# Performance work log

Measured on AMD Instinct MI355X. Metric: run time of the kernel, lower is better.

The kernel has to match this reference:

```python
import jax, jax.numpy as jnp
import numpy as np

NUM_AGES = 100
FEAT_DIM = 512
BATCH = 4096
TEMPERATURE = 0.1
EPS = 1e-6


def setup_inputs() -> dict:
    key = jax.random.key(0)
    k1, k2, k3 = jax.random.split(key, 3)
    z_age = jax.random.normal(k1, (BATCH, FEAT_DIM), dtype=jnp.float32)
    ages = jax.random.randint(k2, (BATCH,), 0, NUM_AGES, dtype=jnp.int64)
    proxies = jax.random.normal(k3, (NUM_AGES, FEAT_DIM), dtype=jnp.float32)
    return {"z_age": z_age, "ages": ages, "proxies": proxies}


def _unit_diff(a, b):
    d = a - b
    return d / (jnp.linalg.norm(d, axis=-1, keepdims=True) + EPS)


def reference(z_age, ages, proxies):
    # Vectorized equivalent of the O(B^2) python double loop.
    # Only pairs with age_i < age_j contribute (age_i > age_j branch is a no-op `...`).
    B = z_age.shape[0]
    A = proxies.shape[0]
    aj = ages.astype(jnp.int32)
    c_cur = proxies[aj]                                   # [B, D]
    c_next = proxies[jnp.minimum(aj + 1, A - 1)]          # [B, D]
    c_prev = proxies[jnp.maximum(aj - 1, 0)]              # [B, D]
    vf = _unit_diff(c_next, c_cur)                        # forward direction per sample j
    vb = _unit_diff(c_prev, c_cur)                        # backward direction per sample j

    # Pairwise norms via Gram matrix: ||z_i - z_j||.
    G = z_age @ z_age.T                                   # [B, B]
    sq = jnp.diagonal(G)                                  # [B]
    d2 = jnp.maximum(sq[:, None] + sq[None, :] - 2.0 * G, 0.0)
    norm = jnp.sqrt(d2)                                   # [B, B]
    denom = norm + EPS

    # dot(v_d_ij, v_f_j) = (z_i . vf_j - z_j . vf_j) / (||z_i - z_j|| + eps)
    Gf = z_age @ vf.T                                     # [B, B], Gf[i, j] = z_i . vf_j
    Gb = z_age @ vb.T
    dot_f = (Gf - jnp.diagonal(Gf)[None, :]) / denom
    dot_b = (Gb - jnp.diagonal(Gb)[None, :]) / denom

    # -log(exp(df/T) / (exp(df/T) + exp(db/T))) = softplus((db - df)/T)
    per_pair = jax.nn.softplus((dot_b - dot_f) / TEMPERATURE)  # [B, B]
    mask = ages[:, None] < ages[None, :]
    loss = jnp.sum(jnp.where(mask, per_pair, 0.0))
    return loss / (B * (B - 1))
```

## Files before the change

### kernel.cpp

```cpp
#include <hip/hip_runtime.h>
#include <hip/hip_bf16.h>

#define NUM_AGES 100
#define FEAT 512
#define BATCH 4096
#define EPSF 1e-6f
#define INV_T 10.0f
#define INV_NORM (1.0f / ((float)BATCH * (float)(BATCH - 1)))

#define BM 128
#define BN 128
#define BK 64
#define NTILES 528

typedef __bf16 bf16_t;
typedef __bf16 v8bf __attribute__((ext_vector_type(8)));
typedef float v4f __attribute__((ext_vector_type(4)));

__device__ __forceinline__ void async16(const void* g, void* l) {
  __builtin_amdgcn_global_load_lds(
      (const __attribute__((address_space(1))) void*)g,
      (__attribute__((address_space(3))) void*)l, 16, 0, 0);
}

__global__ __launch_bounds__(512) void prep_kernel(
    const float* __restrict__ z, const int* __restrict__ ages,
    const float* __restrict__ proxies,
    bf16_t* __restrict__ zb, bf16_t* __restrict__ wb,
    float* __restrict__ sq, float* __restrict__ hd,
    int* __restrict__ ages_s, float* __restrict__ out)
{
  __shared__ __attribute__((aligned(16))) int sa[BATCH];
  int t = threadIdx.x;
  int wv = t >> 6, lane = t & 63;
  if (blockIdx.x == 0 && t == 0) out[0] = 0.0f;

  ((int4*)sa)[t]       = ((const int4*)ages)[t];
  ((int4*)sa)[t + 512] = ((const int4*)ages)[t + 512];
  __syncthreads();

  int j = blockIdx.x * 8 + wv;
  int araw = sa[j];

  int cnt = 0;
  const int4* sa4 = (const int4*)sa;
#pragma unroll
  for (int e = 0; e < 16; ++e) {
    int idx = lane + 64 * e;
    int4 v = sa4[idx];
    int k = idx * 4;
    cnt += (v.x < araw || (v.x == araw && k     < j)) ? 1 : 0;
    cnt += (v.y < araw || (v.y == araw && k + 1 < j)) ? 1 : 0;
    cnt += (v.z < araw || (v.z == araw && k + 2 < j)) ? 1 : 0;
    cnt += (v.w < araw || (v.w == araw && k + 3 < j)) ? 1 : 0;
  }

  int a  = araw < 0 ? 0 : (araw > NUM_AGES - 1 ? NUM_AGES - 1 : araw);
  int an = a + 1 > NUM_AGES - 1 ? NUM_AGES - 1 : a + 1;
  int ap = a - 1 < 0 ? 0 : a - 1;
  int c0 = lane * 8;
  const float4* cc4 = (const float4*)(proxies + (size_t)a  * FEAT + c0);
  const float4* cn4 = (const float4*)(proxies + (size_t)an * FEAT + c0);
  const float4* cp4 = (const float4*)(proxies + (size_t)ap * FEAT + c0);
  const float4* zr4 = (const float4*)(z + (size_t)j * FEAT + c0);

  float zv[8], df[8], db[8];
  float ff = 0.f, bb = 0.f, zz = 0.f, zf = 0.f, zbs = 0.f;
#pragma unroll
  for (int h = 0; h < 2; ++h) {
    float4 c4 = cc4[h], n4 = cn4[h], p4 = cp4[h], z4 = zr4[h];
    float cA[4] = {c4.x, c4.y, c4.z, c4.w};
    float nA[4] = {n4.x, n4.y, n4.z, n4.w};
    float pA[4] = {p4.x, p4.y, p4.z, p4.w};
    float zA[4] = {z4.x, z4.y, z4.z, z4.w};
#pragma unroll
    for (int i2 = 0; i2 < 4; ++i2) {
      int i = h * 4 + i2;
      zv[i] = zA[i2];
      df[i] = nA[i2] - cA[i2];
      db[i] = pA[i2] - cA[i2];
      ff  += df[i] * df[i];
      bb  += db[i] * db[i];
      zz  += zv[i] * zv[i];
      zf  += zv[i] * df[i];
      zbs += zv[i] * db[i];
    }
  }

#pragma unroll
  for (int off = 32; off > 0; off >>= 1) {
    ff  += __shfl_xor(ff,  off, 64);
    bb  += __shfl_xor(bb,  off, 64);
    zz  += __shfl_xor(zz,  off, 64);
    zf  += __shfl_xor(zf,  off, 64);
    zbs += __shfl_xor(zbs, off, 64);
    cnt += __shfl_xor(cnt, off, 64);
  }
  int rank = cnt;
  float rf = 1.0f / (sqrtf(ff) + EPSF);
  float rb = 1.0f / (sqrtf(bb) + EPSF);
  int key = rank & 7;
  int c2s = (c0 & ~63) | ((((c0 >> 3) & 7) ^ key) << 3);

  union { bf16_t h[8]; uint4 u; } uz, uw;
#pragma unroll
  for (int i = 0; i < 8; ++i) {
    uz.h[i] = (bf16_t)zv[i];
    uw.h[i] = (bf16_t)(db[i] * rb - df[i] * rf);
  }
  *(uint4*)((char*)zb + ((size_t)rank * FEAT + c2s) * 2) = uz.u;
  *(uint4*)((char*)wb + ((size_t)rank * FEAT + c2s) * 2) = uw.u;
  if (lane == 0) {
    sq[rank] = zz;
    hd[rank] = rb * zbs - rf * zf;
    ages_s[rank] = araw;
  }
}

__global__ __launch_bounds__(256, 2) void pair_kernel(
    const bf16_t* __restrict__ zb, const bf16_t* __restrict__ wb,
    const float* __restrict__ sq, const float* __restrict__ hd,
    const int* __restrict__ ages, float* __restrict__ out)
{
  __shared__ __attribute__((aligned(16))) char lds[49152];
  __shared__ float s_sqi[BM];
  __shared__ int   s_agei[BM];
  __shared__ float s_sqj[BN];
  __shared__ float s_hdj[BN];
  __shared__ int   s_agej[BN];
  __shared__ float wsum[4];

  int t = threadIdx.x;
  int wv = t >> 6, lane = t & 63;

  int id = (blockIdx.x & 7) * (NTILES / 8) + (blockIdx.x >> 3);
  int bx = 0, rem = id;
  while (rem >= bx + 1) { rem -= bx + 1; ++bx; }
  int by = rem;
  int i0 = by * BM, j0 = bx * BN;

  if (t < BM) {
    s_sqi[t] = sq[i0 + t];
    s_agei[t] = ages[i0 + t];
  } else {
    int u = t - BM;
    s_sqj[u] = sq[j0 + u];
    s_hdj[u] = hd[j0 + u];
    s_agej[u] = ages[j0 + u];
  }

  v4f accG[4][4], accH[4][4];
#pragma unroll
  for (int a = 0; a < 4; ++a)
#pragma unroll
    for (int b = 0; b < 4; ++b) {
      accG[a][b] = (v4f){0.f, 0.f, 0.f, 0.f};
      accH[a][b] = (v4f){0.f, 0.f, 0.f, 0.f};
    }

  int wm = wv >> 1, wn = wv & 1;
  int lm = lane & 15, q = lane >> 4;
  int psw0 = ((q    ) ^ (lm & 7)) * 16;
  int psw1 = ((q + 4) ^ (lm & 7)) * 16;

  int loff = (lane >> 3) * FEAT + (lane & 7) * 8;
  const bf16_t* baseA = zb + (size_t)i0 * FEAT + loff;
  const bf16_t* baseZ = zb + (size_t)j0 * FEAT + loff;
  const bf16_t* baseW = wb + (size_t)j0 * FEAT + loff;

  for (int k0 = 0; k0 < FEAT; k0 += BK) {
#pragma unroll
    for (int c = 0; c < 4; ++c) {
      int chunk = wv * 4 + c;
      async16(baseA + (size_t)chunk * 8 * FEAT + k0, lds + chunk * 1024);
      async16(baseZ + (size_t)chunk * 8 * FEAT + k0, lds + 16384 + chunk * 1024);
      async16(baseW + (size_t)chunk * 8 * FEAT + k0, lds + 32768 + chunk * 1024);
    }
    __syncthreads();

#pragma unroll
    for (int s = 0; s < 2; ++s) {
      int psw = s ? psw1 : psw0;
      v8bf afr[4], bz[4], bw[4];
#pragma unroll
      for (int mi = 0; mi < 4; ++mi) {
        int r = wm * 64 + mi * 16 + lm;
        afr[mi] = *(const v8bf*)(lds + r * 128 + psw);
      }
#pragma unroll
      for (int ni = 0; ni < 4; ++ni) {
        int r = wn * 64 + ni * 16 + lm;
        bz[ni] = *(const v8bf*)(lds + 16384 + r * 128 + psw);
        bw[ni] = *(const v8bf*)(lds + 32768 + r * 128 + psw);
      }
#pragma unroll
      for (int mi = 0; mi < 4; ++mi)
#pragma unroll
        for (int ni = 0; ni < 4; ++ni) {
          accG[mi][ni] = __builtin_amdgcn_mfma_f32_16x16x32_bf16(afr[mi], bz[ni], accG[mi][ni], 0, 0, 0);
          accH[mi][ni] = __builtin_amdgcn_mfma_f32_16x16x32_bf16(afr[mi], bw[ni], accH[mi][ni], 0, 0, 0);
        }
    }
    __syncthreads();
  }

  float tsum = 0.f;
#pragma unroll
  for (int ni = 0; ni < 4; ++ni) {
    int jl = wn * 64 + ni * 16 + lm;
    float sqj = s_sqj[jl];
    float hdj = s_hdj[jl];
    int aj = s_agej[jl];
#pragma unroll
    for (int mi = 0; mi < 4; ++mi) {
#pragma unroll
      for (int r = 0; r < 4; ++r) {
        int il = wm * 64 + mi * 16 + q * 4 + r;
        float g = accG[mi][ni][r];
        float h = accH[mi][ni][r];
        float d2 = fmaxf(s_sqi[il] + sqj - 2.0f * g, 1e-12f);
        float rs = __builtin_amdgcn_rsqf(d2);
        float arg = (h - hdj) * INV_T * rs;
        float sp = fmaxf(arg, 0.0f) + __logf(1.0f + __expf(-fabsf(arg)));
        tsum += (s_agei[il] < aj) ? sp : 0.0f;
      }
    }
  }

#pragma unroll
  for (int off = 32; off > 0; off >>= 1) tsum += __shfl_down(tsum, off, 64);
  if (lane == 0) wsum[wv] = tsum;
  __syncthreads();
  if (t == 0)
    atomicAdd(out, (wsum[0] + wsum[1] + wsum[2] + wsum[3]) * INV_NORM);
}

extern "C" void kernel_launch(void* const* d_in, const int* in_sizes, int n_in,
                              void* d_out, int out_size, void* d_ws, size_t ws_size,
                              hipStream_t stream) {
  const float* z = (const float*)d_in[0];
  const int* ages = (const int*)d_in[1];
  const float* proxies = (const float*)d_in[2];
  float* out = (float*)d_out;

  char* ws = (char*)d_ws;
  bf16_t* zb = (bf16_t*)ws;
  bf16_t* wb = (bf16_t*)(ws + (size_t)4 * 1024 * 1024);
  size_t o = (size_t)8 * 1024 * 1024;
  float* sq      = (float*)(ws + o);
  float* hd      = (float*)(ws + o + 16384);
  int*   ages_s  = (int*)  (ws + o + 32768);

  prep_kernel<<<BATCH / 8, 512, 0, stream>>>(z, ages, proxies, zb, wb, sq, hd, ages_s, out);
  pair_kernel<<<NTILES, 256, 0, stream>>>(zb, wb, sq, hd, ages_s, out);
}
```

Measured before the change: 102.0 us.

## Replace per-sample direction GEMM with small per-age projection table

The second GEMM against per-sample direction vectors is replaced by a small GEMM of z against the 100 per-age direction vectors (padded to 128), producing a [128 x B] fp32 table. The pair kernel then does only the Gram GEMM and looks up h values from that table in its epilogue. This halves MFMA work and LDS traffic in the pair kernel and lets it use fewer registers, allowing 3 blocks per CU. In exchange it adds an extra kernel launch and scattered global reads of the table in the epilogue.

```diff
diff --git a/kernel.cpp b/kernel.cpp
--- a/kernel.cpp
+++ b/kernel.cpp
@@ -12,6 +12,7 @@
 #define BN 128
 #define BK 64
 #define NTILES 528
+#define UROWS 128
 
 typedef __bf16 bf16_t;
 typedef __bf16 v8bf __attribute__((ext_vector_type(8)));
@@ -26,13 +27,59 @@
 __global__ __launch_bounds__(512) void prep_kernel(
     const float* __restrict__ z, const int* __restrict__ ages,
     const float* __restrict__ proxies,
-    bf16_t* __restrict__ zb, bf16_t* __restrict__ wb,
-    float* __restrict__ sq, float* __restrict__ hd,
-    int* __restrict__ ages_s, float* __restrict__ out)
+    bf16_t* __restrict__ zb, bf16_t* __restrict__ ub,
+    float* __restrict__ sq, int* __restrict__ ages_s, float* __restrict__ out)
 {
-  __shared__ __attribute__((aligned(16))) int sa[BATCH];
   int t = threadIdx.x;
   int wv = t >> 6, lane = t & 63;
+
+  if (blockIdx.x >= 512) {
+    int a = (blockIdx.x - 512) * 8 + wv;
+    int c0 = lane * 8;
+    union { bf16_t h[8]; uint4 u; } uw;
+    if (a < NUM_AGES) {
+      int an = a + 1 > NUM_AGES - 1 ? NUM_AGES - 1 : a + 1;
+      int ap = a - 1 < 0 ? 0 : a - 1;
+      const float4* cc4 = (const float4*)(proxies + (size_t)a  * FEAT + c0);
+      const float4* cn4 = (const float4*)(proxies + (size_t)an * FEAT + c0);
+      const float4* cp4 = (const float4*)(proxies + (size_t)ap * FEAT + c0);
+      float df[8], db[8];
+      float ff = 0.f, bb = 0.f;
+#pragma unroll
+      for (int h = 0; h < 2; ++h) {
+        float4 c4 = cc4[h], n4 = cn4[h], p4 = cp4[h];
+        float cA[4] = {c4.x, c4.y, c4.z, c4.w};
+        float nA[4] = {n4.x, n4.y, n4.z, n4.w};
+        float pA[4] = {p4.x, p4.y, p4.z, p4.w};
+#pragma unroll
+        for (int i2 = 0; i2 < 4; ++i2) {
+          int i = h * 4 + i2;
+          df[i] = nA[i2] - cA[i2];
+          db[i] = pA[i2] - cA[i2];
+          ff += df[i] * df[i];
+          bb += db[i] * db[i];
+        }
+      }
+#pragma unroll
+      for (int off = 32; off > 0; off >>= 1) {
+        ff += __shfl_xor(ff, off, 64);
+        bb += __shfl_xor(bb, off, 64);
+      }
+      float rf = 1.0f / (sqrtf(ff) + EPSF);
+      float rb = 1.0f / (sqrtf(bb) + EPSF);
+#pragma unroll
+      for (int i = 0; i < 8; ++i)
+        uw.h[i] = (bf16_t)(db[i] * rb - df[i] * rf);
+    } else {
+      uw.u = (uint4){0u, 0u, 0u, 0u};
+    }
+    int key = a & 7;
+    int c2s = (c0 & ~63) | ((((c0 >> 3) & 7) ^ key) << 3);
+    *(uint4*)((char*)ub + ((size_t)a * FEAT + c2s) * 2) = uw.u;
+    return;
+  }
+
+  __shared__ __attribute__((aligned(16))) int sa[BATCH];
   if (blockIdx.x == 0 && t == 0) out[0] = 0.0f;
 
   ((int4*)sa)[t]       = ((const int4*)ages)[t];
@@ -55,74 +102,110 @@
     cnt += (v.w < araw || (v.w == araw && k + 3 < j)) ? 1 : 0;
   }
 
-  int a  = araw < 0 ? 0 : (araw > NUM_AGES - 1 ? NUM_AGES - 1 : araw);
-  int an = a + 1 > NUM_AGES - 1 ? NUM_AGES - 1 : a + 1;
-  int ap = a - 1 < 0 ? 0 : a - 1;
   int c0 = lane * 8;
-  const float4* cc4 = (const float4*)(proxies + (size_t)a  * FEAT + c0);
-  const float4* cn4 = (const float4*)(proxies + (size_t)an * FEAT + c0);
-  const float4* cp4 = (const float4*)(proxies + (size_t)ap * FEAT + c0);
   const float4* zr4 = (const float4*)(z + (size_t)j * FEAT + c0);
-
-  float zv[8], df[8], db[8];
-  float ff = 0.f, bb = 0.f, zz = 0.f, zf = 0.f, zbs = 0.f;
+  float zv[8];
+  float zz = 0.f;
 #pragma unroll
   for (int h = 0; h < 2; ++h) {
-    float4 c4 = cc4[h], n4 = cn4[h], p4 = cp4[h], z4 = zr4[h];
-    float cA[4] = {c4.x, c4.y, c4.z, c4.w};
-    float nA[4] = {n4.x, n4.y, n4.z, n4.w};
-    float pA[4] = {p4.x, p4.y, p4.z, p4.w};
+    float4 z4 = zr4[h];
     float zA[4] = {z4.x, z4.y, z4.z, z4.w};
 #pragma unroll
     for (int i2 = 0; i2 < 4; ++i2) {
-      int i = h * 4 + i2;
-      zv[i] = zA[i2];
-      df[i] = nA[i2] - cA[i2];
-      db[i] = pA[i2] - cA[i2];
-      ff  += df[i] * df[i];
-      bb  += db[i] * db[i];
-      zz  += zv[i] * zv[i];
-      zf  += zv[i] * df[i];
-      zbs += zv[i] * db[i];
-    }
-  }
-
+      zv[h * 4 + i2] = zA[i2];
+      zz += zA[i2] * zA[i2];
+    }
+  }
 #pragma unroll
   for (int off = 32; off > 0; off >>= 1) {
-    ff  += __shfl_xor(ff,  off, 64);
-    bb  += __shfl_xor(bb,  off, 64);
     zz  += __shfl_xor(zz,  off, 64);
-    zf  += __shfl_xor(zf,  off, 64);
-    zbs += __shfl_xor(zbs, off, 64);
     cnt += __shfl_xor(cnt, off, 64);
   }
   int rank = cnt;
-  float rf = 1.0f / (sqrtf(ff) + EPSF);
-  float rb = 1.0f / (sqrtf(bb) + EPSF);
   int key = rank & 7;
   int c2s = (c0 & ~63) | ((((c0 >> 3) & 7) ^ key) << 3);
 
-  union { bf16_t h[8]; uint4 u; } uz, uw;
-#pragma unroll
-  for (int i = 0; i < 8; ++i) {
-    uz.h[i] = (bf16_t)zv[i];
-    uw.h[i] = (bf16_t)(db[i] * rb - df[i] * rf);
-  }
+  union { bf16_t h[8]; uint4 u; } uz;
+#pragma unroll
+  for (int i = 0; i < 8; ++i) uz.h[i] = (bf16_t)zv[i];
   *(uint4*)((char*)zb + ((size_t)rank * FEAT + c2s) * 2) = uz.u;
-  *(uint4*)((char*)wb + ((size_t)rank * FEAT + c2s) * 2) = uw.u;
   if (lane == 0) {
     sq[rank] = zz;
-    hd[rank] = rb * zbs - rf * zf;
     ages_s[rank] = araw;
   }
 }
 
-__global__ __launch_bounds__(256, 2) void pair_kernel(
-    const bf16_t* __restrict__ zb, const bf16_t* __restrict__ wb,
-    const float* __restrict__ sq, const float* __restrict__ hd,
-    const int* __restrict__ ages, float* __restrict__ out)
+__global__ __launch_bounds__(256, 3) void zu_kernel(
+    const bf16_t* __restrict__ zb, const bf16_t* __restrict__ ub,
+    float* __restrict__ zut)
 {
-  __shared__ __attribute__((aligned(16))) char lds[49152];
+  __shared__ __attribute__((aligned(16))) char lds[32768];
+  int t = threadIdx.x;
+  int wv = t >> 6, lane = t & 63;
+  int r0 = blockIdx.x * 128;
+
+  v4f acc[4][4];
+#pragma unroll
+  for (int a = 0; a < 4; ++a)
+#pragma unroll
+    for (int b = 0; b < 4; ++b) acc[a][b] = (v4f){0.f, 0.f, 0.f, 0.f};
+
+  int wm = wv >> 1, wn = wv & 1;
+  int lm = lane & 15, q = lane >> 4;
+  int psw0 = ((q    ) ^ (lm & 7)) * 16;
+  int psw1 = ((q + 4) ^ (lm & 7)) * 16;
+  int loff = (lane >> 3) * FEAT + (lane & 7) * 8;
+  const bf16_t* baseA = zb + (size_t)r0 * FEAT + loff;
+  const bf16_t* baseU = ub + loff;
+
+  for (int k0 = 0; k0 < FEAT; k0 += BK) {
+#pragma unroll
+    for (int c = 0; c < 4; ++c) {
+      int chunk = wv * 4 + c;
+      async16(baseA + (size_t)chunk * 8 * FEAT + k0, lds + chunk * 1024);
+      async16(baseU + (size_t)chunk * 8 * FEAT + k0, lds + 16384 + chunk * 1024);
+    }
+    __syncthreads();
+#pragma unroll
+    for (int s = 0; s < 2; ++s) {
+      int psw = s ? psw1 : psw0;
+      v8bf afr[4], bu[4];
+#pragma unroll
+      for (int mi = 0; mi < 4; ++mi) {
+        int r = wm * 64 + mi * 16 + lm;
+        afr[mi] = *(const v8bf*)(lds + r * 128 + psw);
+      }
+#pragma unroll
+      for (int ni = 0; ni < 4; ++ni) {
+        int r = wn * 64 + ni * 16 + lm;
+        bu[ni] = *(const v8bf*)(lds + 16384 + r * 128 + psw);
+      }
+#pragma unroll
+      for (int mi = 0; mi < 4; ++mi)
+#pragma unroll
+        for (int ni = 0; ni < 4; ++ni)
+          acc[mi][ni] = __builtin_amdgcn_mfma_f32_16x16x32_bf16(afr[mi], bu[ni], acc[mi][ni], 0, 0, 0);
+    }
+    __syncthreads();
+  }
+
+#pragma unroll
+  for (int ni = 0; ni < 4; ++ni) {
+    int age = wn * 64 + ni * 16 + lm;
+#pragma unroll
+    for (int mi = 0; mi < 4; ++mi) {
+      int rb0 = r0 + wm * 64 + mi * 16 + q * 4;
+      *(v4f*)(zut + (size_t)age * BATCH + rb0) = acc[mi][ni];
+    }
+  }
+}
+
+__global__ __launch_bounds__(256, 3) void pair_kernel(
+    const bf16_t* __restrict__ zb, const float* __restrict__ zut,
+    const float* __restrict__ sq, const int* __restrict__ ages,
+    float* __restrict__ out)
+{
+  __shared__ __attribute__((aligned(16))) char lds[32768];
   __shared__ float s_sqi[BM];
   __shared__ int   s_agei[BM];
   __shared__ float s_sqj[BN];
@@ -144,19 +227,18 @@
     s_agei[t] = ages[i0 + t];
   } else {
     int u = t - BM;
+    int raw = ages[j0 + u];
+    int ac = raw < 0 ? 0 : (raw > NUM_AGES - 1 ? NUM_AGES - 1 : raw);
     s_sqj[u] = sq[j0 + u];
-    s_hdj[u] = hd[j0 + u];
-    s_agej[u] = ages[j0 + u];
-  }
-
-  v4f accG[4][4], accH[4][4];
+    s_agej[u] = raw;
+    s_hdj[u] = zut[(size_t)ac * BATCH + j0 + u];
+  }
+
+  v4f accG[4][4];
 #pragma unroll
   for (int a = 0; a < 4; ++a)
 #pragma unroll
-    for (int b = 0; b < 4; ++b) {
-      accG[a][b] = (v4f){0.f, 0.f, 0.f, 0.f};
-      accH[a][b] = (v4f){0.f, 0.f, 0.f, 0.f};
-    }
+    for (int b = 0; b < 4; ++b) accG[a][b] = (v4f){0.f, 0.f, 0.f, 0.f};
 
   int wm = wv >> 1, wn = wv & 1;
   int lm = lane & 15, q = lane >> 4;
@@ -166,7 +248,6 @@
   int loff = (lane >> 3) * FEAT + (lane & 7) * 8;
   const bf16_t* baseA = zb + (size_t)i0 * FEAT + loff;
   const bf16_t* baseZ = zb + (size_t)j0 * FEAT + loff;
-  const bf16_t* baseW = wb + (size_t)j0 * FEAT + loff;
 
   for (int k0 = 0; k0 < FEAT; k0 += BK) {
 #pragma unroll
@@ -174,14 +255,13 @@
       int chunk = wv * 4 + c;
       async16(baseA + (size_t)chunk * 8 * FEAT + k0, lds + chunk * 1024);
       async16(baseZ + (size_t)chunk * 8 * FEAT + k0, lds + 16384 + chunk * 1024);
-      async16(baseW + (size_t)chunk * 8 * FEAT + k0, lds + 32768 + chunk * 1024);
     }
     __syncthreads();
 
 #pragma unroll
     for (int s = 0; s < 2; ++s) {
       int psw = s ? psw1 : psw0;
-      v8bf afr[4], bz[4], bw[4];
+      v8bf afr[4], bz[4];
 #pragma unroll
       for (int mi = 0; mi < 4; ++mi) {
         int r = wm * 64 + mi * 16 + lm;
@@ -191,15 +271,12 @@
       for (int ni = 0; ni < 4; ++ni) {
         int r = wn * 64 + ni * 16 + lm;
         bz[ni] = *(const v8bf*)(lds + 16384 + r * 128 + psw);
-        bw[ni] = *(const v8bf*)(lds + 32768 + r * 128 + psw);
       }
 #pragma unroll
       for (int mi = 0; mi < 4; ++mi)
 #pragma unroll
-        for (int ni = 0; ni < 4; ++ni) {
+        for (int ni = 0; ni < 4; ++ni)
           accG[mi][ni] = __builtin_amdgcn_mfma_f32_16x16x32_bf16(afr[mi], bz[ni], accG[mi][ni], 0, 0, 0);
-          accH[mi][ni] = __builtin_amdgcn_mfma_f32_16x16x32_bf16(afr[mi], bw[ni], accH[mi][ni], 0, 0, 0);
-        }
     }
     __syncthreads();
   }
@@ -211,16 +288,20 @@
     float sqj = s_sqj[jl];
     float hdj = s_hdj[jl];
     int aj = s_agej[jl];
+    int ac = aj < 0 ? 0 : (aj > NUM_AGES - 1 ? NUM_AGES - 1 : aj);
+    const float* zrow = zut + (size_t)ac * BATCH + i0;
 #pragma unroll
     for (int mi = 0; mi < 4; ++mi) {
+      int ilb = wm * 64 + mi * 16 + q * 4;
+      float4 h4 = *(const float4*)(zrow + ilb);
+      float hh[4] = {h4.x, h4.y, h4.z, h4.w};
 #pragma unroll
       for (int r = 0; r < 4; ++r) {
-        int il = wm * 64 + mi * 16 + q * 4 + r;
+        int il = ilb + r;
         float g = accG[mi][ni][r];
-        float h = accH[mi][ni][r];
         float d2 = fmaxf(s_sqi[il] + sqj - 2.0f * g, 1e-12f);
         float rs = __builtin_amdgcn_rsqf(d2);
-        float arg = (h - hdj) * INV_T * rs;
+        float arg = (hh[r] - hdj) * INV_T * rs;
         float sp = fmaxf(arg, 0.0f) + __logf(1.0f + __expf(-fabsf(arg)));
         tsum += (s_agei[il] < aj) ? sp : 0.0f;
       }
@@ -244,13 +325,13 @@
   float* out = (float*)d_out;
 
   char* ws = (char*)d_ws;
-  bf16_t* zb = (bf16_t*)ws;
-  bf16_t* wb = (bf16_t*)(ws + (size_t)4 * 1024 * 1024);
-  size_t o = (size_t)8 * 1024 * 1024;
-  float* sq      = (float*)(ws + o);
-  float* hd      = (float*)(ws + o + 16384);
-  int*   ages_s  = (int*)  (ws + o + 32768);
-
-  prep_kernel<<<BATCH / 8, 512, 0, stream>>>(z, ages, proxies, zb, wb, sq, hd, ages_s, out);
-  pair_kernel<<<NTILES, 256, 0, stream>>>(zb, wb, sq, hd, ages_s, out);
-}
+  bf16_t* zb  = (bf16_t*)ws;
+  bf16_t* ub  = (bf16_t*)(ws + (size_t)4 * 1024 * 1024);
+  float*  zut = (float*) (ws + (size_t)6 * 1024 * 1024);
+  float*  sq     = (float*)(ws + (size_t)8 * 1024 * 1024);
+  int*    ages_s = (int*)  (ws + (size_t)8 * 1024 * 1024 + 16384);
+
+  prep_kernel<<<528, 512, 0, stream>>>(z, ages, proxies, zb, ub, sq, ages_s, out);
+  zu_kernel<<<32, 256, 0, stream>>>(zb, ub, zut);
+  pair_kernel<<<NTILES, 256, 0, stream>>>(zb, zut, sq, ages_s, out);
+}
```

Result: faster. 96.71 us (-5.2%).
